# Kernel tuning notes

Measured on AMD Instinct MI355X. Metric: run time of the kernel, lower is better.

Reference implementation:

```python
import jax, jax.numpy as jnp
import numpy as np

K = 16
D = 1024
B = 65536

# Row-major off-diagonal index order matching the torch double loop (i, j, i != j)
_ii, _jj = np.nonzero(~np.eye(K, dtype=bool))  # each (K*(K-1),), row-major
OFF_I = jnp.asarray(_ii)
OFF_J = jnp.asarray(_jj)
DIAG = jnp.arange(K)


def setup_inputs() -> dict:
    key = jax.random.key(0)
    k1, k2, k3, k4, k5 = jax.random.split(key, 5)
    scale_d = 1.0 / np.sqrt(D)
    return {
        "x": jax.random.normal(k1, (B, D), dtype=jnp.float32),
        "Wd": jax.random.normal(k2, (K, D), dtype=jnp.float32) * scale_d,
        "bd": jax.random.normal(k3, (K,), dtype=jnp.float32) * 0.1,
        "Wo": jax.random.normal(k4, (K * (K - 1), D), dtype=jnp.float32) * scale_d,
        "bo": jax.random.normal(k5, (K * (K - 1),), dtype=jnp.float32) * 0.1 - 3.0,
    }


def reference(x, Wd, bd, Wo, bo):
    # Diagonal gates: (B, K)
    c_diag = jax.nn.sigmoid(jnp.einsum("bd,kd->bk", x, Wd) + bd)
    # Off-diagonal values: (B, K*(K-1)), non-positive
    off_vals = -jax.nn.softplus(jnp.einsum("bd,kd->bk", x, Wo) + bo)
    C = jnp.zeros((x.shape[0], K, K), dtype=x.dtype)
    C = C.at[:, OFF_I, OFF_J].set(off_vals)
    C = C.at[:, DIAG, DIAG].set(c_diag)
    return C
```

## Files before the change

### kernel.cpp

```cpp
#include <hip/hip_runtime.h>
#include <hip/hip_bf16.h>
#include <stdint.h>


typedef __bf16 bf16x8 __attribute__((ext_vector_type(8)));
typedef float f32x4 __attribute__((ext_vector_type(4)));

#define THREADS 256
#define BM 64
#define KSTEPS 32
#define WIMG 16384
#define WBYTES (WIMG * KSTEPS)

__device__ __forceinline__ unsigned bf_rtne(unsigned u) {
  return (u + 0x7fffu + ((u >> 16) & 1u)) >> 16;
}
__device__ __forceinline__ unsigned pack2(float lo, float hi) {
  return bf_rtne(__float_as_uint(lo)) | (bf_rtne(__float_as_uint(hi)) << 16);
}

__device__ __forceinline__ void gload_lds16(const void* g, void* l) {
  __builtin_amdgcn_global_load_lds(
      (const __attribute__((address_space(1))) unsigned int*)g,
      (__attribute__((address_space(3))) unsigned int*)l, 16, 0, 0);
}

__global__ void prep_kernel(const float* __restrict__ Wd, const float* __restrict__ bd,
                            const float* __restrict__ Wo, const float* __restrict__ bo,
                            char* __restrict__ wbuf, float* __restrict__ bias) {
  const int c = blockIdx.x;
  const int t = threadIdx.x;
  const int i = c >> 4, j = c & 15;
  const float* src;
  float b;
  if (i == j) { src = Wd + i * 1024; b = bd[i]; }
  else { int r = i * 15 + (j < i ? j : j - 1); src = Wo + r * 1024; b = bo[r]; }
  if (t == 0) bias[c] = b;
  const int kk = t * 4;
  const int img = kk >> 5, k5 = kk & 31;
  float4 v = *reinterpret_cast<const float4*>(src + kk);
  uint2 h;
  h.x = pack2(v.x, v.y);
  h.y = pack2(v.z, v.w);
  const unsigned off = (unsigned)((c * 64 + k5 * 2) ^ (((c >> 1) & 3) << 4));
  *reinterpret_cast<uint2*>(wbuf + img * WIMG + off) = h;
}

__global__ __launch_bounds__(THREADS, 4) void cap_main(
    const float* __restrict__ x, const char* __restrict__ wbuf,
    const float* __restrict__ bias, float* __restrict__ out) {
  __shared__ char smem[40960];

  const int tid = threadIdx.x;
  const int wid = tid >> 6;
  const int lane = tid & 63;
  const int l15 = lane & 15;
  const int l4 = lane >> 4;

  const size_t blkRow = (size_t)blockIdx.x * BM;

  const int ar = tid >> 2;
  const int akc = tid & 3;
  const float* xs = x + (blkRow + (size_t)ar) * 1024 + akc * 8;
  const unsigned awz = (unsigned)((ar * 64 + akc * 16) ^ (((ar >> 1) & 3) << 4));

  const unsigned sw = (unsigned)(((l15 >> 1) & 3) << 4);
  const unsigned abase = (unsigned)((l15 * 64 + l4 * 16) ^ sw);
  const unsigned bbase = (unsigned)(((wid * 64 + l15) * 64 + l4 * 16) ^ sw);

  f32x4 acc[4][4];
#pragma unroll
  for (int m = 0; m < 4; ++m)
#pragma unroll
    for (int n = 0; n < 4; ++n) acc[m][n] = (f32x4){0.f, 0.f, 0.f, 0.f};

  {
    float4 p0 = *reinterpret_cast<const float4*>(xs);
    float4 p1 = *reinterpret_cast<const float4*>(xs + 4);
#pragma unroll
    for (int i = 0; i < 4; ++i)
      gload_lds16(wbuf + (wid * 4 + i) * 1024 + lane * 16,
                  smem + 8192 + (wid * 4 + i) * 1024);
    uint4 w;
    w.x = pack2(p0.x, p0.y); w.y = pack2(p0.z, p0.w);
    w.z = pack2(p1.x, p1.y); w.w = pack2(p1.z, p1.w);
    *reinterpret_cast<uint4*>(smem + awz) = w;
  }
  __syncthreads();

  for (int t = 0; t < KSTEPS; ++t) {
    const int cur = t & 1;
    const char* Ac = smem + cur * 4096;
    const char* Bc = smem + 8192 + cur * 16384;
    char* An = smem + (cur ^ 1) * 4096;
    char* Bn = smem + 8192 + (cur ^ 1) * 16384;

    float4 p0, p1;
    if (t + 1 < KSTEPS) {
      const float* xsp = xs + (t + 1) * 32;
      p0 = *reinterpret_cast<const float4*>(xsp);
      p1 = *reinterpret_cast<const float4*>(xsp + 4);
      const char* wsp = wbuf + (t + 1) * WIMG;
#pragma unroll
      for (int i = 0; i < 4; ++i)
        gload_lds16(wsp + (wid * 4 + i) * 1024 + lane * 16, Bn + (wid * 4 + i) * 1024);
    }

    bf16x8 af[4], bfr[4];
#pragma unroll
    for (int m = 0; m < 4; ++m)
      af[m] = *reinterpret_cast<const bf16x8*>(Ac + abase + m * 1024);
#pragma unroll
    for (int n = 0; n < 4; ++n)
      bfr[n] = *reinterpret_cast<const bf16x8*>(Bc + bbase + n * 1024);
#pragma unroll
    for (int m = 0; m < 4; ++m)
#pragma unroll
      for (int n = 0; n < 4; ++n)
        acc[m][n] = __builtin_amdgcn_mfma_f32_16x16x32_bf16(af[m], bfr[n], acc[m][n], 0, 0, 0);

    if (t + 1 < KSTEPS) {
      uint4 w;
      w.x = pack2(p0.x, p0.y); w.y = pack2(p0.z, p0.w);
      w.z = pack2(p1.x, p1.y); w.w = pack2(p1.z, p1.w);
      *reinterpret_cast<uint4*>(An + awz) = w;
    }
    __syncthreads();
  }

  float bs[4];
#pragma unroll
  for (int n = 0; n < 4; ++n) bs[n] = bias[wid * 64 + n * 16 + l15];

  const int rr2 = tid >> 4;
  const int co = (tid & 15) * 16;
  const char* rdp = smem + rr2 * 1040 + co * 4;

#pragma unroll
  for (int p = 0; p < 4; ++p) {
#pragma unroll
    for (int n = 0; n < 4; ++n) {
      const int col = wid * 64 + n * 16 + l15;
      const bool diag = (col % 17) == 0;
#pragma unroll
      for (int j2 = 0; j2 < 4; ++j2) {
        const int rr = l4 * 4 + j2;
        float v = acc[p][n][j2] + bs[n];
        float e = __expf(-fabsf(v));
        float sig = (v >= 0.f) ? 1.f / (1.f + e) : e / (1.f + e);
        float sp = fmaxf(v, 0.f) + __logf(1.f + e);
        *reinterpret_cast<float*>(smem + rr * 1040 + col * 4) = diag ? sig : -sp;
      }
    }
    __syncthreads();
    float4 o0 = *reinterpret_cast<const float4*>(rdp);
    float4 o1 = *reinterpret_cast<const float4*>(rdp + 16);
    float4 o2 = *reinterpret_cast<const float4*>(rdp + 32);
    float4 o3 = *reinterpret_cast<const float4*>(rdp + 48);
    float* orow = out + (blkRow + (size_t)(p * 16 + rr2)) * 256 + co;
    *reinterpret_cast<float4*>(orow) = o0;
    *reinterpret_cast<float4*>(orow + 4) = o1;
    *reinterpret_cast<float4*>(orow + 8) = o2;
    *reinterpret_cast<float4*>(orow + 12) = o3;
    __syncthreads();
  }
}

extern "C" void kernel_launch(void* const* d_in, const int* in_sizes, int n_in,
                              void* d_out, int out_size, void* d_ws, size_t ws_size,
                              hipStream_t stream) {
  const float* x = (const float*)d_in[0];
  const float* Wd = (const float*)d_in[1];
  const float* bd = (const float*)d_in[2];
  const float* Wo = (const float*)d_in[3];
  const float* bo = (const float*)d_in[4];
  float* out = (float*)d_out;
  char* wbuf = (char*)d_ws;
  float* bias = (float*)(wbuf + WBYTES);

  prep_kernel<<<dim3(256), dim3(256), 0, stream>>>(Wd, bd, Wo, bo, wbuf, bias);
  cap_main<<<dim3(1024), dim3(THREADS), 0, stream>>>(x, wbuf, bias, out);
}
```

Measured before the change: 106.7 us.

## Double block tile rows, add 4-stage weight pipeline with manual waitcnt

Raises the block to 512 threads covering 128 rows, with warps arranged 2x4 over M and N, which halves how many times each block reloads the shared weight tiles. Weight tiles now use a four-buffer ring in LDS, prefetched two K-steps ahead with explicit vmcnt/lgkmcnt waits and raw barriers in place of __syncthreads. x rows are register double-buffered. LDS use doubles to 80KB and the block count halves, which may lower occupancy, and the hand-written waitcnt counts are fragile.

Measured after the change: 114.7 us. 1.08x slower.

```diff
diff --git a/kernel.cpp b/kernel.cpp
--- a/kernel.cpp
+++ b/kernel.cpp
@@ -6,11 +6,16 @@
 typedef __bf16 bf16x8 __attribute__((ext_vector_type(8)));
 typedef float f32x4 __attribute__((ext_vector_type(4)));
 
-#define THREADS 256
-#define BM 64
+#define THREADS 512
+#define BM 128
 #define KSTEPS 32
 #define WIMG 16384
 #define WBYTES (WIMG * KSTEPS)
+
+#define A_SZ 8192
+#define B_OFF 16384
+#define B_SZ 16384
+#define SMEM_SZ 81920
 
 __device__ __forceinline__ unsigned bf_rtne(unsigned u) {
   return (u + 0x7fffu + ((u >> 16) & 1u)) >> 16;
@@ -49,13 +54,15 @@
 __global__ __launch_bounds__(THREADS, 4) void cap_main(
     const float* __restrict__ x, const char* __restrict__ wbuf,
     const float* __restrict__ bias, float* __restrict__ out) {
-  __shared__ char smem[40960];
+  __shared__ char smem[SMEM_SZ];
 
   const int tid = threadIdx.x;
   const int wid = tid >> 6;
   const int lane = tid & 63;
   const int l15 = lane & 15;
   const int l4 = lane >> 4;
+  const int wm = wid >> 2;
+  const int wn = wid & 3;
 
   const size_t blkRow = (size_t)blockIdx.x * BM;
 
@@ -65,8 +72,8 @@
   const unsigned awz = (unsigned)((ar * 64 + akc * 16) ^ (((ar >> 1) & 3) << 4));
 
   const unsigned sw = (unsigned)(((l15 >> 1) & 3) << 4);
-  const unsigned abase = (unsigned)((l15 * 64 + l4 * 16) ^ sw);
-  const unsigned bbase = (unsigned)(((wid * 64 + l15) * 64 + l4 * 16) ^ sw);
+  const unsigned abase = (unsigned)(((wm * 64 + l15) * 64 + l4 * 16) ^ sw);
+  const unsigned bbase = (unsigned)(((wn * 64 + l15) * 64 + l4 * 16) ^ sw);
 
   f32x4 acc[4][4];
 #pragma unroll
@@ -74,94 +81,108 @@
 #pragma unroll
     for (int n = 0; n < 4; ++n) acc[m][n] = (f32x4){0.f, 0.f, 0.f, 0.f};
 
+  float4 xr[2][2];
+
+  float4 x0a = *reinterpret_cast<const float4*>(xs);
+  float4 x0b = *reinterpret_cast<const float4*>(xs + 4);
+  gload_lds16(wbuf + tid * 16, smem + B_OFF + tid * 16);
+  gload_lds16(wbuf + 8192 + tid * 16, smem + B_OFF + 8192 + tid * 16);
+  gload_lds16(wbuf + WIMG + tid * 16, smem + B_OFF + B_SZ + tid * 16);
+  gload_lds16(wbuf + WIMG + 8192 + tid * 16, smem + B_OFF + B_SZ + 8192 + tid * 16);
+  xr[1][0] = *reinterpret_cast<const float4*>(xs + 32);
+  xr[1][1] = *reinterpret_cast<const float4*>(xs + 36);
+  asm volatile("s_waitcnt vmcnt(4)" ::: "memory");
   {
-    float4 p0 = *reinterpret_cast<const float4*>(xs);
-    float4 p1 = *reinterpret_cast<const float4*>(xs + 4);
-#pragma unroll
-    for (int i = 0; i < 4; ++i)
-      gload_lds16(wbuf + (wid * 4 + i) * 1024 + lane * 16,
-                  smem + 8192 + (wid * 4 + i) * 1024);
     uint4 w;
-    w.x = pack2(p0.x, p0.y); w.y = pack2(p0.z, p0.w);
-    w.z = pack2(p1.x, p1.y); w.w = pack2(p1.z, p1.w);
+    w.x = pack2(x0a.x, x0a.y); w.y = pack2(x0a.z, x0a.w);
+    w.z = pack2(x0b.x, x0b.y); w.w = pack2(x0b.z, x0b.w);
     *reinterpret_cast<uint4*>(smem + awz) = w;
   }
+  asm volatile("s_waitcnt lgkmcnt(0)" ::: "memory");
+  __builtin_amdgcn_s_barrier();
+
+  for (int kk = 0; kk < KSTEPS / 4; ++kk) {
+#pragma unroll
+    for (int i = 0; i < 4; ++i) {
+      const int t = kk * 4 + i;
+      const char* Ac = smem + (i & 1) * A_SZ;
+      const char* Bc = smem + B_OFF + i * B_SZ;
+      char* Aw = smem + ((i + 1) & 1) * A_SZ;
+      char* Bw = smem + B_OFF + ((i + 2) & 3) * B_SZ;
+
+      bf16x8 af[4], bfr[4];
+#pragma unroll
+      for (int m = 0; m < 4; ++m)
+        af[m] = *reinterpret_cast<const bf16x8*>(Ac + abase + m * 1024);
+#pragma unroll
+      for (int n = 0; n < 4; ++n)
+        bfr[n] = *reinterpret_cast<const bf16x8*>(Bc + bbase + n * 1024);
+
+      const int tB = (t + 2 < KSTEPS) ? t + 2 : KSTEPS - 1;
+      const char* wsp = wbuf + tB * WIMG;
+      gload_lds16(wsp + tid * 16, Bw + tid * 16);
+      gload_lds16(wsp + 8192 + tid * 16, Bw + 8192 + tid * 16);
+      const float* xsp = xs + tB * 32;
+      xr[i & 1][0] = *reinterpret_cast<const float4*>(xsp);
+      xr[i & 1][1] = *reinterpret_cast<const float4*>(xsp + 4);
+
+#pragma unroll
+      for (int m = 0; m < 4; ++m)
+#pragma unroll
+        for (int n = 0; n < 4; ++n)
+          acc[m][n] = __builtin_amdgcn_mfma_f32_16x16x32_bf16(af[m], bfr[n], acc[m][n], 0, 0, 0);
+
+      asm volatile("s_waitcnt vmcnt(4)" ::: "memory");
+
+      {
+        const float4 pa = xr[(i + 1) & 1][0];
+        const float4 pb = xr[(i + 1) & 1][1];
+        uint4 w;
+        w.x = pack2(pa.x, pa.y); w.y = pack2(pa.z, pa.w);
+        w.z = pack2(pb.x, pb.y); w.w = pack2(pb.z, pb.w);
+        *reinterpret_cast<uint4*>(Aw + awz) = w;
+      }
+
+      asm volatile("s_waitcnt lgkmcnt(0)" ::: "memory");
+      __builtin_amdgcn_s_barrier();
+    }
+  }
+
+  float bs[4];
+#pragma unroll
+  for (int n = 0; n < 4; ++n) bs[n] = bias[wn * 64 + n * 16 + l15];
+
+  const int rr2 = tid >> 5;
+  const int co = (tid & 31) * 8;
+  const char* rdp = smem + rr2 * 1040 + co * 4;
+
   __syncthreads();
 
-  for (int t = 0; t < KSTEPS; ++t) {
-    const int cur = t & 1;
-    const char* Ac = smem + cur * 4096;
-    const char* Bc = smem + 8192 + cur * 16384;
-    char* An = smem + (cur ^ 1) * 4096;
-    char* Bn = smem + 8192 + (cur ^ 1) * 16384;
-
-    float4 p0, p1;
-    if (t + 1 < KSTEPS) {
-      const float* xsp = xs + (t + 1) * 32;
-      p0 = *reinterpret_cast<const float4*>(xsp);
-      p1 = *reinterpret_cast<const float4*>(xsp + 4);
-      const char* wsp = wbuf + (t + 1) * WIMG;
-#pragma unroll
-      for (int i = 0; i < 4; ++i)
-        gload_lds16(wsp + (wid * 4 + i) * 1024 + lane * 16, Bn + (wid * 4 + i) * 1024);
-    }
-
-    bf16x8 af[4], bfr[4];
-#pragma unroll
-    for (int m = 0; m < 4; ++m)
-      af[m] = *reinterpret_cast<const bf16x8*>(Ac + abase + m * 1024);
-#pragma unroll
-    for (int n = 0; n < 4; ++n)
-      bfr[n] = *reinterpret_cast<const bf16x8*>(Bc + bbase + n * 1024);
-#pragma unroll
-    for (int m = 0; m < 4; ++m)
-#pragma unroll
-      for (int n = 0; n < 4; ++n)
-        acc[m][n] = __builtin_amdgcn_mfma_f32_16x16x32_bf16(af[m], bfr[n], acc[m][n], 0, 0, 0);
-
-    if (t + 1 < KSTEPS) {
-      uint4 w;
-      w.x = pack2(p0.x, p0.y); w.y = pack2(p0.z, p0.w);
-      w.z = pack2(p1.x, p1.y); w.w = pack2(p1.z, p1.w);
-      *reinterpret_cast<uint4*>(An + awz) = w;
-    }
-    __syncthreads();
-  }
-
-  float bs[4];
-#pragma unroll
-  for (int n = 0; n < 4; ++n) bs[n] = bias[wid * 64 + n * 16 + l15];
-
-  const int rr2 = tid >> 4;
-  const int co = (tid & 15) * 16;
-  const char* rdp = smem + rr2 * 1040 + co * 4;
-
-#pragma unroll
-  for (int p = 0; p < 4; ++p) {
-#pragma unroll
-    for (int n = 0; n < 4; ++n) {
-      const int col = wid * 64 + n * 16 + l15;
-      const bool diag = (col % 17) == 0;
-#pragma unroll
-      for (int j2 = 0; j2 < 4; ++j2) {
-        const int rr = l4 * 4 + j2;
-        float v = acc[p][n][j2] + bs[n];
-        float e = __expf(-fabsf(v));
-        float sig = (v >= 0.f) ? 1.f / (1.f + e) : e / (1.f + e);
-        float sp = fmaxf(v, 0.f) + __logf(1.f + e);
-        *reinterpret_cast<float*>(smem + rr * 1040 + col * 4) = diag ? sig : -sp;
+#pragma unroll
+  for (int p = 0; p < 8; ++p) {
+    if ((wid >> 2) == (p >> 2)) {
+      const int m = p & 3;
+#pragma unroll
+      for (int n = 0; n < 4; ++n) {
+        const int col = wn * 64 + n * 16 + l15;
+        const bool diag = (col % 17) == 0;
+#pragma unroll
+        for (int j2 = 0; j2 < 4; ++j2) {
+          const int rr = l4 * 4 + j2;
+          float v = acc[m][n][j2] + bs[n];
+          float e = __expf(-fabsf(v));
+          float sig = (v >= 0.f) ? 1.f / (1.f + e) : e / (1.f + e);
+          float sp = fmaxf(v, 0.f) + __logf(1.f + e);
+          *reinterpret_cast<float*>(smem + rr * 1040 + col * 4) = diag ? sig : -sp;
+        }
       }
     }
     __syncthreads();
     float4 o0 = *reinterpret_cast<const float4*>(rdp);
     float4 o1 = *reinterpret_cast<const float4*>(rdp + 16);
-    float4 o2 = *reinterpret_cast<const float4*>(rdp + 32);
-    float4 o3 = *reinterpret_cast<const float4*>(rdp + 48);
     float* orow = out + (blkRow + (size_t)(p * 16 + rr2)) * 256 + co;
     *reinterpret_cast<float4*>(orow) = o0;
     *reinterpret_cast<float4*>(orow + 4) = o1;
-    *reinterpret_cast<float4*>(orow + 8) = o2;
-    *reinterpret_cast<float4*>(orow + 12) = o3;
     __syncthreads();
   }
 }
@@ -179,5 +200,5 @@
   float* bias = (float*)(wbuf + WBYTES);
 
   prep_kernel<<<dim3(256), dim3(256), 0, stream>>>(Wd, bd, Wo, bo, wbuf, bias);
-  cap_main<<<dim3(1024), dim3(THREADS), 0, stream>>>(x, wbuf, bias, out);
-}
+  cap_main<<<dim3(512), dim3(THREADS), 0, stream>>>(x, wbuf, bias, out);
+}
```

## Load x fragments directly into registers and widen block tile to 128 rows

Applied to the files above, without the earlier changes.

Restructures the GEMM so each wave owns 16 rows of x across all 256 output columns. x is loaded straight from global into MFMA A-fragments instead of being staged through LDS. The block grows to 512 threads and 128 rows, and the K loop uses 64-wide chunks with double-buffered weight tiles, which halves the number of barriers. Each weight tile is reused by twice as many rows, but the change drops to 512 blocks, uses 64KB of LDS, and raises per-wave register use with 16 accumulators.

Result: slower. 109.2 us (+2.4%).

```diff
diff --git a/kernel.cpp b/kernel.cpp
--- a/kernel.cpp
+++ b/kernel.cpp
@@ -6,11 +6,11 @@
 typedef __bf16 bf16x8 __attribute__((ext_vector_type(8)));
 typedef float f32x4 __attribute__((ext_vector_type(4)));
 
-#define THREADS 256
-#define BM 64
-#define KSTEPS 32
-#define WIMG 16384
-#define WBYTES (WIMG * KSTEPS)
+#define THREADS 512
+#define BM 128
+#define NCHUNK 16
+#define CIMG 32768
+#define WBYTES (CIMG * NCHUNK)
 
 __device__ __forceinline__ unsigned bf_rtne(unsigned u) {
   return (u + 0x7fffu + ((u >> 16) & 1u)) >> 16;
@@ -37,19 +37,26 @@
   else { int r = i * 15 + (j < i ? j : j - 1); src = Wo + r * 1024; b = bo[r]; }
   if (t == 0) bias[c] = b;
   const int kk = t * 4;
-  const int img = kk >> 5, k5 = kk & 31;
+  const int chunk = kk >> 6, k6 = kk & 63;
   float4 v = *reinterpret_cast<const float4*>(src + kk);
   uint2 h;
   h.x = pack2(v.x, v.y);
   h.y = pack2(v.z, v.w);
-  const unsigned off = (unsigned)((c * 64 + k5 * 2) ^ (((c >> 1) & 3) << 4));
-  *reinterpret_cast<uint2*>(wbuf + img * WIMG + off) = h;
+  const unsigned off = (unsigned)((c * 128 + k6 * 2) ^ ((c & 7) << 4));
+  *reinterpret_cast<uint2*>(wbuf + chunk * CIMG + off) = h;
+}
+
+__device__ __forceinline__ bf16x8 packfrag(const float4& a, const float4& b) {
+  uint4 u;
+  u.x = pack2(a.x, a.y); u.y = pack2(a.z, a.w);
+  u.z = pack2(b.x, b.y); u.w = pack2(b.z, b.w);
+  return *reinterpret_cast<bf16x8*>(&u);
 }
 
 __global__ __launch_bounds__(THREADS, 4) void cap_main(
     const float* __restrict__ x, const char* __restrict__ wbuf,
     const float* __restrict__ bias, float* __restrict__ out) {
-  __shared__ char smem[40960];
+  __shared__ char smem[65536];
 
   const int tid = threadIdx.x;
   const int wid = tid >> 6;
@@ -59,97 +66,104 @@
 
   const size_t blkRow = (size_t)blockIdx.x * BM;
 
-  const int ar = tid >> 2;
-  const int akc = tid & 3;
-  const float* xs = x + (blkRow + (size_t)ar) * 1024 + akc * 8;
-  const unsigned awz = (unsigned)((ar * 64 + akc * 16) ^ (((ar >> 1) & 3) << 4));
+  const float* xrow = x + (blkRow + (size_t)(wid * 16 + l15)) * 1024 + l4 * 8;
 
-  const unsigned sw = (unsigned)(((l15 >> 1) & 3) << 4);
-  const unsigned abase = (unsigned)((l15 * 64 + l4 * 16) ^ sw);
-  const unsigned bbase = (unsigned)(((wid * 64 + l15) * 64 + l4 * 16) ^ sw);
+  const unsigned swz = (unsigned)((l15 & 7) << 4);
+  const unsigned ds0 = (unsigned)(l15 * 128 + ((l4 * 16) ^ swz));
+  const unsigned ds1 = (unsigned)(l15 * 128 + ((64 + l4 * 16) ^ swz));
 
-  f32x4 acc[4][4];
+  f32x4 acc[16];
 #pragma unroll
-  for (int m = 0; m < 4; ++m)
+  for (int n = 0; n < 16; ++n) acc[n] = (f32x4){0.f, 0.f, 0.f, 0.f};
+
+  float4 p0, p1, p2, p3;
+
 #pragma unroll
-    for (int n = 0; n < 4; ++n) acc[m][n] = (f32x4){0.f, 0.f, 0.f, 0.f};
+  for (int i = 0; i < 4; ++i)
+    gload_lds16(wbuf + i * 8192 + tid * 16, smem + i * 8192 + tid * 16);
+  asm volatile("" ::: "memory");
+  p0 = *reinterpret_cast<const float4*>(xrow);
+  p1 = *reinterpret_cast<const float4*>(xrow + 4);
+  p2 = *reinterpret_cast<const float4*>(xrow + 32);
+  p3 = *reinterpret_cast<const float4*>(xrow + 36);
+  asm volatile("s_waitcnt vmcnt(0)" ::: "memory");
+  __builtin_amdgcn_s_barrier();
+
+#define COMPUTE(BUF, AF0, AF1)                                                  \
+  {                                                                             \
+    _Pragma("unroll") for (int ks = 0; ks < 2; ++ks) {                          \
+      const char* bp = (BUF) + (ks ? ds1 : ds0);                                \
+      const bf16x8 a = ks ? (AF1) : (AF0);                                      \
+      _Pragma("unroll") for (int n0 = 0; n0 < 16; n0 += 4) {                    \
+        bf16x8 b0 = *reinterpret_cast<const bf16x8*>(bp + (n0 + 0) * 2048);     \
+        bf16x8 b1 = *reinterpret_cast<const bf16x8*>(bp + (n0 + 1) * 2048);     \
+        bf16x8 b2 = *reinterpret_cast<const bf16x8*>(bp + (n0 + 2) * 2048);     \
+        bf16x8 b3 = *reinterpret_cast<const bf16x8*>(bp + (n0 + 3) * 2048);     \
+        acc[n0 + 0] = __builtin_amdgcn_mfma_f32_16x16x32_bf16(a, b0, acc[n0 + 0], 0, 0, 0); \
+        acc[n0 + 1] = __builtin_amdgcn_mfma_f32_16x16x32_bf16(a, b1, acc[n0 + 1], 0, 0, 0); \
+        acc[n0 + 2] = __builtin_amdgcn_mfma_f32_16x16x32_bf16(a, b2, acc[n0 + 2], 0, 0, 0); \
+        acc[n0 + 3] = __builtin_amdgcn_mfma_f32_16x16x32_bf16(a, b3, acc[n0 + 3], 0, 0, 0); \
+      }                                                                         \
+    }                                                                           \
+  }
+
+  for (int c = 0; c < NCHUNK - 1; ++c) {
+    const char* Bc = smem + (c & 1) * 32768;
+    char* Bn = smem + ((c + 1) & 1) * 32768;
+
+    bf16x8 af0 = packfrag(p0, p1);
+    bf16x8 af1 = packfrag(p2, p3);
+
+    const char* wsp = wbuf + (c + 1) * CIMG;
+#pragma unroll
+    for (int i = 0; i < 4; ++i)
+      gload_lds16(wsp + i * 8192 + tid * 16, Bn + i * 8192 + tid * 16);
+    asm volatile("" ::: "memory");
+    const float* xp = xrow + (c + 1) * 64;
+    p0 = *reinterpret_cast<const float4*>(xp);
+    p1 = *reinterpret_cast<const float4*>(xp + 4);
+    p2 = *reinterpret_cast<const float4*>(xp + 32);
+    p3 = *reinterpret_cast<const float4*>(xp + 36);
+    asm volatile("" ::: "memory");
+
+    COMPUTE(Bc, af0, af1);
+
+    asm volatile("s_waitcnt vmcnt(4)" ::: "memory");
+    asm volatile("s_waitcnt lgkmcnt(0)" ::: "memory");
+    __builtin_amdgcn_s_barrier();
+  }
 
   {
-    float4 p0 = *reinterpret_cast<const float4*>(xs);
-    float4 p1 = *reinterpret_cast<const float4*>(xs + 4);
-#pragma unroll
-    for (int i = 0; i < 4; ++i)
-      gload_lds16(wbuf + (wid * 4 + i) * 1024 + lane * 16,
-                  smem + 8192 + (wid * 4 + i) * 1024);
-    uint4 w;
-    w.x = pack2(p0.x, p0.y); w.y = pack2(p0.z, p0.w);
-    w.z = pack2(p1.x, p1.y); w.w = pack2(p1.z, p1.w);
-    *reinterpret_cast<uint4*>(smem + awz) = w;
+    bf16x8 af0 = packfrag(p0, p1);
+    bf16x8 af1 = packfrag(p2, p3);
+    const char* Bc = smem + ((NCHUNK - 1) & 1) * 32768;
+    COMPUTE(Bc, af0, af1);
   }
-  __syncthreads();
+  asm volatile("s_waitcnt lgkmcnt(0)" ::: "memory");
+  __builtin_amdgcn_s_barrier();
 
-  for (int t = 0; t < KSTEPS; ++t) {
-    const int cur = t & 1;
-    const char* Ac = smem + cur * 4096;
-    const char* Bc = smem + 8192 + cur * 16384;
-    char* An = smem + (cur ^ 1) * 4096;
-    char* Bn = smem + 8192 + (cur ^ 1) * 16384;
-
-    float4 p0, p1;
-    if (t + 1 < KSTEPS) {
-      const float* xsp = xs + (t + 1) * 32;
-      p0 = *reinterpret_cast<const float4*>(xsp);
-      p1 = *reinterpret_cast<const float4*>(xsp + 4);
-      const char* wsp = wbuf + (t + 1) * WIMG;
-#pragma unroll
-      for (int i = 0; i < 4; ++i)
-        gload_lds16(wsp + (wid * 4 + i) * 1024 + lane * 16, Bn + (wid * 4 + i) * 1024);
-    }
-
-    bf16x8 af[4], bfr[4];
-#pragma unroll
-    for (int m = 0; m < 4; ++m)
-      af[m] = *reinterpret_cast<const bf16x8*>(Ac + abase + m * 1024);
-#pragma unroll
-    for (int n = 0; n < 4; ++n)
-      bfr[n] = *reinterpret_cast<const bf16x8*>(Bc + bbase + n * 1024);
-#pragma unroll
-    for (int m = 0; m < 4; ++m)
-#pragma unroll
-      for (int n = 0; n < 4; ++n)
-        acc[m][n] = __builtin_amdgcn_mfma_f32_16x16x32_bf16(af[m], bfr[n], acc[m][n], 0, 0, 0);
-
-    if (t + 1 < KSTEPS) {
-      uint4 w;
-      w.x = pack2(p0.x, p0.y); w.y = pack2(p0.z, p0.w);
-      w.z = pack2(p1.x, p1.y); w.w = pack2(p1.z, p1.w);
-      *reinterpret_cast<uint4*>(An + awz) = w;
-    }
-    __syncthreads();
-  }
-
-  float bs[4];
-#pragma unroll
-  for (int n = 0; n < 4; ++n) bs[n] = bias[wid * 64 + n * 16 + l15];
-
-  const int rr2 = tid >> 4;
-  const int co = (tid & 15) * 16;
-  const char* rdp = smem + rr2 * 1040 + co * 4;
+  const int err = tid >> 4;
+  const int ec = tid & 15;
+  const char* rdp = smem + err * 1040 + ec * 64;
 
 #pragma unroll
   for (int p = 0; p < 4; ++p) {
+    if ((wid >> 1) == p) {
+      const int sr = (wid & 1) * 16;
 #pragma unroll
-    for (int n = 0; n < 4; ++n) {
-      const int col = wid * 64 + n * 16 + l15;
-      const bool diag = (col % 17) == 0;
+      for (int n = 0; n < 16; ++n) {
+        const int col = n * 16 + l15;
+        const float bv = bias[col];
+        const bool diag = (col % 17) == 0;
 #pragma unroll
-      for (int j2 = 0; j2 < 4; ++j2) {
-        const int rr = l4 * 4 + j2;
-        float v = acc[p][n][j2] + bs[n];
-        float e = __expf(-fabsf(v));
-        float sig = (v >= 0.f) ? 1.f / (1.f + e) : e / (1.f + e);
-        float sp = fmaxf(v, 0.f) + __logf(1.f + e);
-        *reinterpret_cast<float*>(smem + rr * 1040 + col * 4) = diag ? sig : -sp;
+        for (int j2 = 0; j2 < 4; ++j2) {
+          float v = acc[n][j2] + bv;
+          float e = __expf(-fabsf(v));
+          float sig = (v >= 0.f) ? 1.f / (1.f + e) : e / (1.f + e);
+          float sp = fmaxf(v, 0.f) + __logf(1.f + e);
+          *reinterpret_cast<float*>(smem + (sr + l4 * 4 + j2) * 1040 + col * 4) =
+              diag ? sig : -sp;
+        }
       }
     }
     __syncthreads();
@@ -157,7 +171,7 @@
     float4 o1 = *reinterpret_cast<const float4*>(rdp + 16);
     float4 o2 = *reinterpret_cast<const float4*>(rdp + 32);
     float4 o3 = *reinterpret_cast<const float4*>(rdp + 48);
-    float* orow = out + (blkRow + (size_t)(p * 16 + rr2)) * 256 + co;
+    float* orow = out + (blkRow + (size_t)(p * 32 + err)) * 256 + ec * 16;
     *reinterpret_cast<float4*>(orow) = o0;
     *reinterpret_cast<float4*>(orow + 4) = o1;
     *reinterpret_cast<float4*>(orow + 8) = o2;
@@ -179,5 +193,5 @@
   float* bias = (float*)(wbuf + WBYTES);
 
   prep_kernel<<<dim3(256), dim3(256), 0, stream>>>(Wd, bd, Wo, bo, wbuf, bias);
-  cap_main<<<dim3(1024), dim3(THREADS), 0, stream>>>(x, wbuf, bias, out);
+  cap_main<<<dim3(512), dim3(THREADS), 0, stream>>>(x, wbuf, bias, out);
 }
```

## Load GEMM operands directly from global into registers, dropping LDS staging

Applied to the files above, without the earlier changes.

The main loop no longer stages x and the packed weights through double-buffered shared memory with barriers. Instead each wave reads the x rows and the pre-swizzled bf16 weight fragments straight from global memory into MFMA-ready registers. The prep kernel now lays out weights so each lane's 16-byte fragment is contiguous. Shared memory shrinks to the epilogue buffer and launch bounds drop to 2 blocks per SM to make room for more registers. In exchange, the four waves of a block each re-read the same x rows from global/L2, and per-lane x loads are strided rather than coalesced.

Result: slower. 215.4 us (+101.8%).

```diff
diff --git a/kernel.cpp b/kernel.cpp
--- a/kernel.cpp
+++ b/kernel.cpp
@@ -8,9 +8,9 @@
 
 #define THREADS 256
 #define BM 64
-#define KSTEPS 32
-#define WIMG 16384
-#define WBYTES (WIMG * KSTEPS)
+#define NCHUNK 16
+#define CIMG 32768
+#define WBYTES (CIMG * NCHUNK)
 
 __device__ __forceinline__ unsigned bf_rtne(unsigned u) {
   return (u + 0x7fffu + ((u >> 16) & 1u)) >> 16;
@@ -18,11 +18,11 @@
 __device__ __forceinline__ unsigned pack2(float lo, float hi) {
   return bf_rtne(__float_as_uint(lo)) | (bf_rtne(__float_as_uint(hi)) << 16);
 }
-
-__device__ __forceinline__ void gload_lds16(const void* g, void* l) {
-  __builtin_amdgcn_global_load_lds(
-      (const __attribute__((address_space(1))) unsigned int*)g,
-      (__attribute__((address_space(3))) unsigned int*)l, 16, 0, 0);
+__device__ __forceinline__ bf16x8 packfrag(const float4& a, const float4& b) {
+  uint4 u;
+  u.x = pack2(a.x, a.y); u.y = pack2(a.z, a.w);
+  u.z = pack2(b.x, b.y); u.w = pack2(b.z, b.w);
+  return *reinterpret_cast<bf16x8*>(&u);
 }
 
 __global__ void prep_kernel(const float* __restrict__ Wd, const float* __restrict__ bd,
@@ -37,19 +37,18 @@
   else { int r = i * 15 + (j < i ? j : j - 1); src = Wo + r * 1024; b = bo[r]; }
   if (t == 0) bias[c] = b;
   const int kk = t * 4;
-  const int img = kk >> 5, k5 = kk & 31;
+  const int ch = kk >> 6, ks = (kk >> 5) & 1, q = (kk >> 3) & 3, e = kk & 7;
   float4 v = *reinterpret_cast<const float4*>(src + kk);
   uint2 h;
   h.x = pack2(v.x, v.y);
   h.y = pack2(v.z, v.w);
-  const unsigned off = (unsigned)((c * 64 + k5 * 2) ^ (((c >> 1) & 3) << 4));
-  *reinterpret_cast<uint2*>(wbuf + img * WIMG + off) = h;
+  *reinterpret_cast<uint2*>(wbuf + ch * CIMG + ks * 16384 + q * 4096 + c * 16 + e * 2) = h;
 }
 
-__global__ __launch_bounds__(THREADS, 4) void cap_main(
+__global__ __launch_bounds__(THREADS, 2) void cap_main(
     const float* __restrict__ x, const char* __restrict__ wbuf,
     const float* __restrict__ bias, float* __restrict__ out) {
-  __shared__ char smem[40960];
+  __shared__ char smem[16640];
 
   const int tid = threadIdx.x;
   const int wid = tid >> 6;
@@ -59,14 +58,8 @@
 
   const size_t blkRow = (size_t)blockIdx.x * BM;
 
-  const int ar = tid >> 2;
-  const int akc = tid & 3;
-  const float* xs = x + (blkRow + (size_t)ar) * 1024 + akc * 8;
-  const unsigned awz = (unsigned)((ar * 64 + akc * 16) ^ (((ar >> 1) & 3) << 4));
-
-  const unsigned sw = (unsigned)(((l15 >> 1) & 3) << 4);
-  const unsigned abase = (unsigned)((l15 * 64 + l4 * 16) ^ sw);
-  const unsigned bbase = (unsigned)(((wid * 64 + l15) * 64 + l4 * 16) ^ sw);
+  const float* xb = x + (blkRow + (size_t)l15) * 1024 + l4 * 8;
+  const char* wb = wbuf + l4 * 4096 + (wid * 64 + l15) * 16;
 
   f32x4 acc[4][4];
 #pragma unroll
@@ -74,67 +67,47 @@
 #pragma unroll
     for (int n = 0; n < 4; ++n) acc[m][n] = (f32x4){0.f, 0.f, 0.f, 0.f};
 
-  {
-    float4 p0 = *reinterpret_cast<const float4*>(xs);
-    float4 p1 = *reinterpret_cast<const float4*>(xs + 4);
+#pragma unroll 2
+  for (int ch = 0; ch < NCHUNK; ++ch) {
+    uint4 bu[2][4];
 #pragma unroll
-    for (int i = 0; i < 4; ++i)
-      gload_lds16(wbuf + (wid * 4 + i) * 1024 + lane * 16,
-                  smem + 8192 + (wid * 4 + i) * 1024);
-    uint4 w;
-    w.x = pack2(p0.x, p0.y); w.y = pack2(p0.z, p0.w);
-    w.z = pack2(p1.x, p1.y); w.w = pack2(p1.z, p1.w);
-    *reinterpret_cast<uint4*>(smem + awz) = w;
-  }
-  __syncthreads();
+    for (int ks = 0; ks < 2; ++ks)
+#pragma unroll
+      for (int n = 0; n < 4; ++n)
+        bu[ks][n] = *reinterpret_cast<const uint4*>(
+            wb + ch * CIMG + ks * 16384 + n * 256);
 
-  for (int t = 0; t < KSTEPS; ++t) {
-    const int cur = t & 1;
-    const char* Ac = smem + cur * 4096;
-    const char* Bc = smem + 8192 + cur * 16384;
-    char* An = smem + (cur ^ 1) * 4096;
-    char* Bn = smem + 8192 + (cur ^ 1) * 16384;
-
-    float4 p0, p1;
-    if (t + 1 < KSTEPS) {
-      const float* xsp = xs + (t + 1) * 32;
-      p0 = *reinterpret_cast<const float4*>(xsp);
-      p1 = *reinterpret_cast<const float4*>(xsp + 4);
-      const char* wsp = wbuf + (t + 1) * WIMG;
-#pragma unroll
-      for (int i = 0; i < 4; ++i)
-        gload_lds16(wsp + (wid * 4 + i) * 1024 + lane * 16, Bn + (wid * 4 + i) * 1024);
-    }
-
-    bf16x8 af[4], bfr[4];
-#pragma unroll
-    for (int m = 0; m < 4; ++m)
-      af[m] = *reinterpret_cast<const bf16x8*>(Ac + abase + m * 1024);
-#pragma unroll
-    for (int n = 0; n < 4; ++n)
-      bfr[n] = *reinterpret_cast<const bf16x8*>(Bc + bbase + n * 1024);
+    float4 ax[4][2][2];
 #pragma unroll
     for (int m = 0; m < 4; ++m)
 #pragma unroll
-      for (int n = 0; n < 4; ++n)
-        acc[m][n] = __builtin_amdgcn_mfma_f32_16x16x32_bf16(af[m], bfr[n], acc[m][n], 0, 0, 0);
+      for (int ks = 0; ks < 2; ++ks) {
+        const float* p = xb + (size_t)m * 16384 + ch * 64 + ks * 32;
+        ax[m][ks][0] = *reinterpret_cast<const float4*>(p);
+        ax[m][ks][1] = *reinterpret_cast<const float4*>(p + 4);
+      }
 
-    if (t + 1 < KSTEPS) {
-      uint4 w;
-      w.x = pack2(p0.x, p0.y); w.y = pack2(p0.z, p0.w);
-      w.z = pack2(p1.x, p1.y); w.w = pack2(p1.z, p1.w);
-      *reinterpret_cast<uint4*>(An + awz) = w;
-    }
-    __syncthreads();
+#pragma unroll
+    for (int ks = 0; ks < 2; ++ks)
+#pragma unroll
+      for (int m = 0; m < 4; ++m) {
+        bf16x8 af = packfrag(ax[m][ks][0], ax[m][ks][1]);
+#pragma unroll
+        for (int n = 0; n < 4; ++n)
+          acc[m][n] = __builtin_amdgcn_mfma_f32_16x16x32_bf16(
+              af, *reinterpret_cast<const bf16x8*>(&bu[ks][n]), acc[m][n], 0, 0, 0);
+      }
   }
 
-  float bs[4];
+  float bv[4];
 #pragma unroll
-  for (int n = 0; n < 4; ++n) bs[n] = bias[wid * 64 + n * 16 + l15];
+  for (int n = 0; n < 4; ++n) bv[n] = bias[wid * 64 + n * 16 + l15];
 
-  const int rr2 = tid >> 4;
-  const int co = (tid & 15) * 16;
-  const char* rdp = smem + rr2 * 1040 + co * 4;
+  const int rr = tid >> 4;
+  const int cg = tid & 15;
+  const char* rdp = smem + rr * 1040 + cg * 64;
+
+  __syncthreads();
 
 #pragma unroll
   for (int p = 0; p < 4; ++p) {
@@ -144,12 +117,12 @@
       const bool diag = (col % 17) == 0;
 #pragma unroll
       for (int j2 = 0; j2 < 4; ++j2) {
-        const int rr = l4 * 4 + j2;
-        float v = acc[p][n][j2] + bs[n];
+        float v = acc[p][n][j2] + bv[n];
         float e = __expf(-fabsf(v));
         float sig = (v >= 0.f) ? 1.f / (1.f + e) : e / (1.f + e);
         float sp = fmaxf(v, 0.f) + __logf(1.f + e);
-        *reinterpret_cast<float*>(smem + rr * 1040 + col * 4) = diag ? sig : -sp;
+        *reinterpret_cast<float*>(smem + (l4 * 4 + j2) * 1040 + col * 4) =
+            diag ? sig : -sp;
       }
     }
     __syncthreads();
@@ -157,7 +130,7 @@
     float4 o1 = *reinterpret_cast<const float4*>(rdp + 16);
     float4 o2 = *reinterpret_cast<const float4*>(rdp + 32);
     float4 o3 = *reinterpret_cast<const float4*>(rdp + 48);
-    float* orow = out + (blkRow + (size_t)(p * 16 + rr2)) * 256 + co;
+    float* orow = out + (blkRow + (size_t)(p * 16 + rr)) * 256 + cg * 16;
     *reinterpret_cast<float4*>(orow) = o0;
     *reinterpret_cast<float4*>(orow + 4) = o1;
     *reinterpret_cast<float4*>(orow + 8) = o2;
```
